# Kernel optimization log

Measured on AMD Instinct MI355X. Metric: run time of the kernel, lower is better.

Reference implementation:

```python
import jax, jax.numpy as jnp
import numpy as np


def setup_inputs() -> dict:
    key = jax.random.key(0)
    ks = jax.random.split(key, 7)
    B, S, D, R = 4, 4096, 1024, 16
    scale = 1.0 / np.sqrt(D)
    return {
        "x": jax.random.normal(ks[0], (B, S, D), dtype=jnp.float32),
        "W_qkv": jax.random.normal(ks[1], (3 * D, D), dtype=jnp.float32) * scale,
        "b_qkv": jax.random.normal(ks[2], (3 * D,), dtype=jnp.float32) * 0.02,
        "W_a_q": jax.random.normal(ks[3], (R, D), dtype=jnp.float32) * scale,
        "W_b_q": jnp.zeros((D, R), dtype=jnp.float32) + jax.random.normal(ks[4], (D, R), dtype=jnp.float32) * 0.02,
        "W_a_v": jax.random.normal(ks[5], (R, D), dtype=jnp.float32) * scale,
        "W_b_v": jax.random.normal(ks[6], (D, R), dtype=jnp.float32) * 0.02,
    }


def reference(x, W_qkv, b_qkv, W_a_q, W_b_q, W_a_v, W_b_v):
    D = W_a_q.shape[1]
    # base qkv projection: [B, S, 3D]
    qkv = jnp.einsum("bsd,ed->bse", x, W_qkv) + b_qkv
    # LoRA branches: x -> [B,S,r] -> [B,S,D]
    q_ba = jnp.einsum("bsr,dr->bsd", jnp.einsum("bsd,rd->bsr", x, W_a_q), W_b_q)
    v_ba = jnp.einsum("bsr,dr->bsd", jnp.einsum("bsd,rd->bsr", x, W_a_v), W_b_v)
    # add into q slice ([:D]) and v slice ([-D:])
    qkv = qkv.at[:, :, :D].add(q_ba)
    qkv = qkv.at[:, :, -D:].add(v_ba)
    return qkv
```

## Files before the change

### kernel.cpp

```cpp
#include <hip/hip_runtime.h>
#include <hip/hip_bf16.h>

typedef __bf16 bf16x4 __attribute__((ext_vector_type(4)));
typedef __bf16 bf16x8 __attribute__((ext_vector_type(8)));
typedef float floatx4 __attribute__((ext_vector_type(4)));

#define GLD16(gp, lp) __builtin_amdgcn_global_load_lds(                      \
    (const __attribute__((address_space(1))) void*)(gp),                     \
    (__attribute__((address_space(3))) void*)(lp), 16, 0, 0)

constexpr int Mdim = 16384;
constexpr int Ndim = 3072;
constexpr int Kdim = 1024;

static __device__ __forceinline__ bf16x8 cvt8(floatx4 lo, floatx4 hi) {
    bf16x8 r;
#pragma unroll
    for (int e = 0; e < 4; ++e) { r[e] = (__bf16)lo[e]; r[e + 4] = (__bf16)hi[e]; }
    return r;
}


__global__ __launch_bounds__(256) void build_weff(
    const float* __restrict__ Wqkv,
    const float* __restrict__ Waq,
    const float* __restrict__ Wbq,
    const float* __restrict__ Wav,
    const float* __restrict__ Wbv,
    __hip_bfloat16* __restrict__ Weff)
{
    const int idx = (blockIdx.x * 256 + threadIdx.x) * 4;
    const int e = idx >> 10;
    const int d = idx & 1023;
    floatx4 v = *(const floatx4*)(Wqkv + idx);
    if (e < 1024) {
#pragma unroll
        for (int r = 0; r < 16; ++r) {
            const float wb = Wbq[e * 16 + r];
            floatx4 wa = *(const floatx4*)(Waq + r * 1024 + d);
#pragma unroll
            for (int q = 0; q < 4; ++q) v[q] += wb * wa[q];
        }
    } else if (e >= 2048) {
        const int e2 = e - 2048;
#pragma unroll
        for (int r = 0; r < 16; ++r) {
            const float wb = Wbv[e2 * 16 + r];
            floatx4 wa = *(const floatx4*)(Wav + r * 1024 + d);
#pragma unroll
            for (int q = 0; q < 4; ++q) v[q] += wb * wa[q];
        }
    }
    bf16x4 o;
#pragma unroll
    for (int q = 0; q < 4; ++q) o[q] = (__bf16)v[q];
    *(bf16x4*)(Weff + idx) = o;
}

__global__ __launch_bounds__(256) void cvt_x(
    const float* __restrict__ x, __hip_bfloat16* __restrict__ xb)
{
    const size_t idx = ((size_t)blockIdx.x * 256 + threadIdx.x) * 8;
    bf16x8 r = cvt8(*(const floatx4*)(x + idx), *(const floatx4*)(x + idx + 4));
    *(bf16x8*)(xb + idx) = r;
}

__global__ __launch_bounds__(512, 2) void gemm_bf16_8ph(
    const __hip_bfloat16* __restrict__ A,
    const __hip_bfloat16* __restrict__ Bw,
    const float* __restrict__ bias,
    float* __restrict__ C)
{
    constexpr int NT = Kdim / 64;
    __shared__ __hip_bfloat16 lds[2][2][256 * 64];

    const int t    = threadIdx.x;
    const int wid  = t >> 6;
    const int lane = t & 63;
    const int wm   = wid >> 2;
    const int wn   = wid & 3;

    constexpr int NWG = (Mdim / 256) * (Ndim / 256);
    const int bid = (blockIdx.x & 7) * (NWG >> 3) + (blockIdx.x >> 3);
    const int bx  = bid % (Ndim / 256);
    const int by  = bid / (Ndim / 256);
    const int m0  = by * 256;
    const int n0  = bx * 256;

    const int srow0 = t >> 3;
    const int scb_s = ((t & 7) * 16) ^ ((srow0 & 7) << 4);

#define STAGE_HALF(G, R0, h, nb_, mat, kt_) do {                               \
    const __hip_bfloat16* _g = (G) + (size_t)((R0) + (h) * 128 + srow0) * Kdim \
                               + (kt_) * 64 + (scb_s >> 1);                    \
    char* _l = (char*)&lds[nb_][mat][0] + (h) * 16384 + t * 16;                \
    GLD16(_g, _l);                                                             \
    GLD16(_g + (size_t)64 * Kdim, _l + 8192);                                  \
} while (0)

    const int fm   = lane & 15;
    const int fk2  = (lane >> 4) * 16;
    const int fxor = (fm & 7) << 4;
    const int cbs0 = fk2 ^ fxor;
    const int cbs1 = (64 + fk2) ^ fxor;

    floatx4 acc[8][4];
#pragma unroll
    for (int i = 0; i < 8; ++i)
#pragma unroll
        for (int j = 0; j < 4; ++j)
            acc[i][j] = (floatx4){0.f, 0.f, 0.f, 0.f};

#define MFMA_QUAD(mq, nq, BQ)                                                  \
    __builtin_amdgcn_s_setprio(1);                                             \
    _Pragma("unroll")                                                          \
    for (int i = 0; i < 4; ++i)                                                \
        _Pragma("unroll")                                                      \
        for (int j = 0; j < 2; ++j) {                                          \
            acc[(mq) * 4 + i][(nq) * 2 + j] =                                  \
                __builtin_amdgcn_mfma_f32_16x16x32_bf16(                       \
                    aq[i][0], BQ[j][0], acc[(mq) * 4 + i][(nq) * 2 + j], 0, 0, 0); \
            acc[(mq) * 4 + i][(nq) * 2 + j] =                                  \
                __builtin_amdgcn_mfma_f32_16x16x32_bf16(                       \
                    aq[i][1], BQ[j][1], acc[(mq) * 4 + i][(nq) * 2 + j], 0, 0, 0); \
        }                                                                      \
    __builtin_amdgcn_s_setprio(0);

    STAGE_HALF(A,  m0, 0, 0, 0, 0);
    STAGE_HALF(A,  m0, 1, 0, 0, 0);
    STAGE_HALF(Bw, n0, 0, 0, 1, 0);
    STAGE_HALF(Bw, n0, 1, 0, 1, 0);

    bf16x8 aq[4][2], bq0[2][2], bq1[2][2];

    for (int kt = 0; kt < NT; ++kt) {
        const int nb = kt & 1;
        const char* Ab = (const char*)&lds[nb][0][0];
        const char* Bb = (const char*)&lds[nb][1][0];

#define LDA8(i, mq, kk) (*(const bf16x8*)(Ab + ((wm * 128 + (mq) * 64 + (i) * 16 + fm) * 128 + cbs##kk)))
#define LDB8(j, nq, kk) (*(const bf16x8*)(Bb + ((wn * 64 + (nq) * 32 + (j) * 16 + fm) * 128 + cbs##kk)))

        if (kt + 1 < NT) {
            STAGE_HALF(A,  m0, 0, nb ^ 1, 0, kt + 1);
            STAGE_HALF(Bw, n0, 0, nb ^ 1, 1, kt + 1);
            asm volatile("s_waitcnt vmcnt(4)" ::: "memory");
        } else {
            asm volatile("s_waitcnt vmcnt(0)" ::: "memory");
        }
        __builtin_amdgcn_s_barrier();
#pragma unroll
        for (int i = 0; i < 4; ++i) { aq[i][0] = LDA8(i, 0, 0); aq[i][1] = LDA8(i, 0, 1); }
#pragma unroll
        for (int j = 0; j < 2; ++j) { bq0[j][0] = LDB8(j, 0, 0); bq0[j][1] = LDB8(j, 0, 1); }
        MFMA_QUAD(0, 0, bq0)
        __builtin_amdgcn_s_barrier();

#pragma unroll
        for (int j = 0; j < 2; ++j) { bq1[j][0] = LDB8(j, 1, 0); bq1[j][1] = LDB8(j, 1, 1); }
        if (kt + 1 < NT) STAGE_HALF(A, m0, 1, nb ^ 1, 0, kt + 1);
        __builtin_amdgcn_s_barrier();
        MFMA_QUAD(0, 1, bq1)
        __builtin_amdgcn_s_barrier();

#pragma unroll
        for (int i = 0; i < 4; ++i) { aq[i][0] = LDA8(i, 1, 0); aq[i][1] = LDA8(i, 1, 1); }
        if (kt + 1 < NT) STAGE_HALF(Bw, n0, 1, nb ^ 1, 1, kt + 1);
        __builtin_amdgcn_s_barrier();
        MFMA_QUAD(1, 0, bq0)
        __builtin_amdgcn_s_barrier();

        MFMA_QUAD(1, 1, bq1)
        __builtin_amdgcn_s_barrier();

#undef LDA8
#undef LDB8
    }

    const int cn = lane & 15;
    const int cm = (lane >> 4) * 4;
    float bv[4];
#pragma unroll
    for (int j = 0; j < 4; ++j)
        bv[j] = bias[n0 + wn * 64 + j * 16 + cn];

#pragma unroll
    for (int mi = 0; mi < 8; ++mi) {
        const int m = m0 + wm * 128 + mi * 16 + cm;
#pragma unroll
        for (int ni = 0; ni < 4; ++ni) {
            const int n = n0 + wn * 64 + ni * 16 + cn;
            const size_t base = (size_t)m * Ndim + n;
#pragma unroll
            for (int r = 0; r < 4; ++r)
                C[base + (size_t)r * Ndim] = acc[mi][ni][r] + bv[ni];
        }
    }
#undef STAGE_HALF
#undef MFMA_QUAD
}


__global__ __launch_bounds__(256, 2) void gemm_bias_f32(
    const float* __restrict__ A, const float* __restrict__ Bw,
    const float* __restrict__ bias, float* __restrict__ C)
{
    constexpr int TK = 32;
    __shared__ __hip_bfloat16 As[128 * TK];
    __shared__ __hip_bfloat16 Bs[128 * TK];

    const int t    = threadIdx.x;
    const int wave = t >> 6;
    const int lane = t & 63;
    const int bx   = blockIdx.x % (Ndim / 128);
    const int by   = blockIdx.x / (Ndim / 128);
    const int m0   = by * 128;
    const int n0   = bx * 128;
    const int wm   = wave >> 1;
    const int wn   = wave & 1;
    const int srow = wave * 16 + (lane >> 2);
    const int scol = (lane & 3) * 8;

    const float* Ag0 = A  + (size_t)(m0 + srow) * Kdim + scol;
    const float* Ag1 = Ag0 + (size_t)64 * Kdim;
    const float* Bg0 = Bw + (size_t)(n0 + srow) * Kdim + scol;
    const float* Bg1 = Bg0 + (size_t)64 * Kdim;

    __hip_bfloat16* Al0 = &As[srow * TK + scol];
    __hip_bfloat16* Al1 = &As[(srow + 64) * TK + scol];
    __hip_bfloat16* Bl0 = &Bs[srow * TK + scol];
    __hip_bfloat16* Bl1 = &Bs[(srow + 64) * TK + scol];

    const int fm = lane & 15;
    const int fk = (lane >> 4) * 8;

    floatx4 acc[4][4];
#pragma unroll
    for (int i = 0; i < 4; ++i)
#pragma unroll
        for (int j = 0; j < 4; ++j)
            acc[i][j] = (floatx4){0.f, 0.f, 0.f, 0.f};

    for (int kt = 0; kt < Kdim; kt += TK) {
        bf16x8 a0 = cvt8(*(const floatx4*)(Ag0 + kt), *(const floatx4*)(Ag0 + kt + 4));
        bf16x8 a1 = cvt8(*(const floatx4*)(Ag1 + kt), *(const floatx4*)(Ag1 + kt + 4));
        bf16x8 b0 = cvt8(*(const floatx4*)(Bg0 + kt), *(const floatx4*)(Bg0 + kt + 4));
        bf16x8 b1 = cvt8(*(const floatx4*)(Bg1 + kt), *(const floatx4*)(Bg1 + kt + 4));
        __syncthreads();
        *(bf16x8*)Al0 = a0;
        *(bf16x8*)Al1 = a1;
        *(bf16x8*)Bl0 = b0;
        *(bf16x8*)Bl1 = b1;
        __syncthreads();

        bf16x8 af[4], bfr[4];
#pragma unroll
        for (int i = 0; i < 4; ++i) {
            af[i]  = *(const bf16x8*)&As[(wm * 64 + i * 16 + fm) * TK + fk];
            bfr[i] = *(const bf16x8*)&Bs[(wn * 64 + i * 16 + fm) * TK + fk];
        }
#pragma unroll
        for (int i = 0; i < 4; ++i)
#pragma unroll
            for (int j = 0; j < 4; ++j)
                acc[i][j] = __builtin_amdgcn_mfma_f32_16x16x32_bf16(af[i], bfr[j], acc[i][j], 0, 0, 0);
    }

    const int cn = lane & 15;
    const int cm = (lane >> 4) * 4;
    float bv[4];
#pragma unroll
    for (int j = 0; j < 4; ++j)
        bv[j] = bias[n0 + wn * 64 + j * 16 + cn];
#pragma unroll
    for (int i = 0; i < 4; ++i) {
        const int m = m0 + wm * 64 + i * 16 + cm;
#pragma unroll
        for (int j = 0; j < 4; ++j) {
            const int n = n0 + wn * 64 + j * 16 + cn;
            const size_t base = (size_t)m * Ndim + n;
#pragma unroll
            for (int r = 0; r < 4; ++r)
                C[base + (size_t)r * Ndim] = acc[i][j][r] + bv[j];
        }
    }
}

__global__ __launch_bounds__(256) void lora_rmw(
    const float* __restrict__ x,
    const float* __restrict__ Waq, const float* __restrict__ Wbq,
    const float* __restrict__ Wav, const float* __restrict__ Wbv,
    float* __restrict__ out)
{
    __shared__ float Pq[64][16];
    __shared__ float Pv[64][16];
    const int t  = threadIdx.x;
    const int m0 = blockIdx.x * 64;
    {
        const int row = t >> 2;
        const int r0  = (t & 3) * 4;
        float accq[4] = {0.f, 0.f, 0.f, 0.f};
        float accv[4] = {0.f, 0.f, 0.f, 0.f};
        const float* xr = x + (size_t)(m0 + row) * Kdim;
        for (int d = 0; d < Kdim; d += 4) {
            floatx4 xv = *(const floatx4*)(xr + d);
#pragma unroll
            for (int rr = 0; rr < 4; ++rr) {
                floatx4 wq = *(const floatx4*)(Waq + (size_t)(r0 + rr) * Kdim + d);
                floatx4 wv = *(const floatx4*)(Wav + (size_t)(r0 + rr) * Kdim + d);
#pragma unroll
                for (int e = 0; e < 4; ++e) {
                    accq[rr] += xv[e] * wq[e];
                    accv[rr] += xv[e] * wv[e];
                }
            }
        }
#pragma unroll
        for (int rr = 0; rr < 4; ++rr) {
            Pq[row][r0 + rr] = accq[rr];
            Pv[row][r0 + rr] = accv[rr];
        }
    }
    __syncthreads();
    const int col  = t * 8;
    const bool isq = col < 1024;
    const int nn0  = isq ? col : col - 1024;
    const int n    = isq ? col : col + 1024;
    const float* Wb = isq ? Wbq : Wbv;
    for (int row = 0; row < 64; ++row) {
        const float* P = isq ? Pq[row] : Pv[row];
        const size_t off = (size_t)(m0 + row) * Ndim + n;
        floatx4 o0 = *(const floatx4*)(out + off);
        floatx4 o1 = *(const floatx4*)(out + off + 4);
#pragma unroll
        for (int i = 0; i < 8; ++i) {
            floatx4 w0 = *(const floatx4*)(Wb + (size_t)(nn0 + i) * 16);
            floatx4 w1 = *(const floatx4*)(Wb + (size_t)(nn0 + i) * 16 + 4);
            floatx4 w2 = *(const floatx4*)(Wb + (size_t)(nn0 + i) * 16 + 8);
            floatx4 w3 = *(const floatx4*)(Wb + (size_t)(nn0 + i) * 16 + 12);
            float s = 0.f;
#pragma unroll
            for (int r = 0; r < 4; ++r)
                s += P[r] * w0[r] + P[r + 4] * w1[r] + P[r + 8] * w2[r] + P[r + 12] * w3[r];
            if (i < 4) o0[i] += s; else o1[i - 4] += s;
        }
        *(floatx4*)(out + off)     = o0;
        *(floatx4*)(out + off + 4) = o1;
    }
}

extern "C" void kernel_launch(void* const* d_in, const int* in_sizes, int n_in,
                              void* d_out, int out_size, void* d_ws, size_t ws_size,
                              hipStream_t stream)
{
    (void)in_sizes; (void)n_in; (void)out_size;
    const float* x    = (const float*)d_in[0];
    const float* Wqkv = (const float*)d_in[1];
    const float* bqkv = (const float*)d_in[2];
    const float* Waq  = (const float*)d_in[3];
    const float* Wbq  = (const float*)d_in[4];
    const float* Wav  = (const float*)d_in[5];
    const float* Wbv  = (const float*)d_in[6];
    float* out = (float*)d_out;

    const size_t WEFF_BYTES = (size_t)Ndim * Kdim * sizeof(__hip_bfloat16);
    const size_t XB_BYTES   = (size_t)Mdim * Kdim * sizeof(__hip_bfloat16);

    if (ws_size >= WEFF_BYTES + XB_BYTES) {
        __hip_bfloat16* Weff = (__hip_bfloat16*)d_ws;
        __hip_bfloat16* xb   = (__hip_bfloat16*)((char*)d_ws + WEFF_BYTES);
        build_weff<<<(Ndim * Kdim / 4) / 256, 256, 0, stream>>>(Wqkv, Waq, Wbq, Wav, Wbv, Weff);
        cvt_x<<<(int)(((size_t)Mdim * Kdim / 8) / 256), 256, 0, stream>>>(x, xb);
        gemm_bf16_8ph<<<(Mdim / 256) * (Ndim / 256), 512, 0, stream>>>(xb, Weff, bqkv, out);
    } else {
        gemm_bias_f32<<<(Mdim / 128) * (Ndim / 128), 256, 0, stream>>>(x, Wqkv, bqkv, out);
        lora_rmw<<<Mdim / 64, 256, 0, stream>>>(x, Waq, Wbq, Wav, Wbv, out);
    }
}
```

Baseline: 366.9 us.

## Restructure GEMM main loop to prefetch B/A halves two stages ahead with fewer barriers

```diff
diff --git a/kernel.cpp b/kernel.cpp
--- a/kernel.cpp
+++ b/kernel.cpp
@@ -65,14 +65,14 @@
     *(bf16x8*)(xb + idx) = r;
 }
 
-__global__ __launch_bounds__(512, 2) void gemm_bf16_8ph(
+__global__ __launch_bounds__(512, 2) void gemm_bf16_v6(
     const __hip_bfloat16* __restrict__ A,
     const __hip_bfloat16* __restrict__ Bw,
     const float* __restrict__ bias,
     float* __restrict__ C)
 {
     constexpr int NT = Kdim / 64;
-    __shared__ __hip_bfloat16 lds[2][2][256 * 64];
+    __shared__ __align__(16) char smem[131072];
 
     const int t    = threadIdx.x;
     const int wid  = t >> 6;
@@ -88,21 +88,23 @@
     const int n0  = bx * 256;
 
     const int srow0 = t >> 3;
-    const int scb_s = ((t & 7) * 16) ^ ((srow0 & 7) << 4);
-
-#define STAGE_HALF(G, R0, h, nb_, mat, kt_) do {                               \
-    const __hip_bfloat16* _g = (G) + (size_t)((R0) + (h) * 128 + srow0) * Kdim \
-                               + (kt_) * 64 + (scb_s >> 1);                    \
-    char* _l = (char*)&lds[nb_][mat][0] + (h) * 16384 + t * 16;                \
-    GLD16(_g, _l);                                                             \
+    const int scb   = ((t & 7) * 16) ^ ((srow0 & 7) << 4);
+    const __hip_bfloat16* Ag = A  + (size_t)(m0 + srow0) * Kdim + (scb >> 1);
+    const __hip_bfloat16* Bg = Bw + (size_t)(n0 + srow0) * Kdim + (scb >> 1);
+
+#define STG(mat, h, kt_, b_) do {                                              \
+    const __hip_bfloat16* _g = ((mat) ? Bg : Ag)                               \
+        + (size_t)((h) * 128) * Kdim + (kt_) * 64;                             \
+    char* _l = smem + (b_) * 65536 + (mat) * 32768 + (h) * 16384 + t * 16;     \
+    GLD16(_g,                     _l);                                         \
     GLD16(_g + (size_t)64 * Kdim, _l + 8192);                                  \
 } while (0)
 
-    const int fm   = lane & 15;
-    const int fk2  = (lane >> 4) * 16;
-    const int fxor = (fm & 7) << 4;
-    const int cbs0 = fk2 ^ fxor;
-    const int cbs1 = (64 + fk2) ^ fxor;
+    const int fm  = lane & 15;
+    const int fk2 = (lane >> 4) * 16;
+    const int fx  = (fm & 7) << 4;
+    const int cb0 = fk2 ^ fx;
+    const int cb1 = (64 + fk2) ^ fx;
 
     floatx4 acc[8][4];
 #pragma unroll
@@ -111,7 +113,7 @@
         for (int j = 0; j < 4; ++j)
             acc[i][j] = (floatx4){0.f, 0.f, 0.f, 0.f};
 
-#define MFMA_QUAD(mq, nq, BQ)                                                  \
+#define MFMA_Q(mq, nq, BQ)                                                     \
     __builtin_amdgcn_s_setprio(1);                                             \
     _Pragma("unroll")                                                          \
     for (int i = 0; i < 4; ++i)                                                \
@@ -119,62 +121,69 @@
         for (int j = 0; j < 2; ++j) {                                          \
             acc[(mq) * 4 + i][(nq) * 2 + j] =                                  \
                 __builtin_amdgcn_mfma_f32_16x16x32_bf16(                       \
-                    aq[i][0], BQ[j][0], acc[(mq) * 4 + i][(nq) * 2 + j], 0, 0, 0); \
+                    aq[i][0], BQ[j][0], acc[(mq) * 4 + i][(nq) * 2 + j], 0,0,0);\
             acc[(mq) * 4 + i][(nq) * 2 + j] =                                  \
                 __builtin_amdgcn_mfma_f32_16x16x32_bf16(                       \
-                    aq[i][1], BQ[j][1], acc[(mq) * 4 + i][(nq) * 2 + j], 0, 0, 0); \
+                    aq[i][1], BQ[j][1], acc[(mq) * 4 + i][(nq) * 2 + j], 0,0,0);\
         }                                                                      \
     __builtin_amdgcn_s_setprio(0);
 
-    STAGE_HALF(A,  m0, 0, 0, 0, 0);
-    STAGE_HALF(A,  m0, 1, 0, 0, 0);
-    STAGE_HALF(Bw, n0, 0, 0, 1, 0);
-    STAGE_HALF(Bw, n0, 1, 0, 1, 0);
+    STG(0, 0, 0, 0); STG(0, 1, 0, 0); STG(1, 0, 0, 0); STG(1, 1, 0, 0);
+    STG(1, 0, 1, 1); STG(0, 0, 1, 1);
 
     bf16x8 aq[4][2], bq0[2][2], bq1[2][2];
 
     for (int kt = 0; kt < NT; ++kt) {
-        const int nb = kt & 1;
-        const char* Ab = (const char*)&lds[nb][0][0];
-        const char* Bb = (const char*)&lds[nb][1][0];
-
-#define LDA8(i, mq, kk) (*(const bf16x8*)(Ab + ((wm * 128 + (mq) * 64 + (i) * 16 + fm) * 128 + cbs##kk)))
-#define LDB8(j, nq, kk) (*(const bf16x8*)(Bb + ((wn * 64 + (nq) * 32 + (j) * 16 + fm) * 128 + cbs##kk)))
+        const int b = kt & 1;
+        const char* Ab = smem + b * 65536;
+        const char* Bb = Ab + 32768;
 
         if (kt + 1 < NT) {
-            STAGE_HALF(A,  m0, 0, nb ^ 1, 0, kt + 1);
-            STAGE_HALF(Bw, n0, 0, nb ^ 1, 1, kt + 1);
-            asm volatile("s_waitcnt vmcnt(4)" ::: "memory");
+            STG(0, 1, kt + 1, b ^ 1);
+            asm volatile("s_waitcnt vmcnt(6)" ::: "memory");
         } else {
             asm volatile("s_waitcnt vmcnt(0)" ::: "memory");
         }
         __builtin_amdgcn_s_barrier();
-#pragma unroll
-        for (int i = 0; i < 4; ++i) { aq[i][0] = LDA8(i, 0, 0); aq[i][1] = LDA8(i, 0, 1); }
-#pragma unroll
-        for (int j = 0; j < 2; ++j) { bq0[j][0] = LDB8(j, 0, 0); bq0[j][1] = LDB8(j, 0, 1); }
-        MFMA_QUAD(0, 0, bq0)
+        __builtin_amdgcn_sched_barrier(0x8);
+#pragma unroll
+        for (int i = 0; i < 4; ++i) {
+            const char* ar = Ab + (wm * 128 + i * 16 + fm) * 128;
+            aq[i][0] = *(const bf16x8*)(ar + cb0);
+            aq[i][1] = *(const bf16x8*)(ar + cb1);
+        }
+#pragma unroll
+        for (int j = 0; j < 2; ++j) {
+            const char* br = Bb + (wn * 64 + j * 16 + fm) * 128;
+            bq0[j][0] = *(const bf16x8*)(br + cb0);
+            bq0[j][1] = *(const bf16x8*)(br + cb1);
+        }
+        MFMA_Q(0, 0, bq0)
+
+#pragma unroll
+        for (int j = 0; j < 2; ++j) {
+            const char* br = Bb + (wn * 64 + 32 + j * 16 + fm) * 128;
+            bq1[j][0] = *(const bf16x8*)(br + cb0);
+            bq1[j][1] = *(const bf16x8*)(br + cb1);
+        }
+        if (kt + 1 < NT) STG(1, 1, kt + 1, b ^ 1);
+        MFMA_Q(0, 1, bq1)
         __builtin_amdgcn_s_barrier();
-
-#pragma unroll
-        for (int j = 0; j < 2; ++j) { bq1[j][0] = LDB8(j, 1, 0); bq1[j][1] = LDB8(j, 1, 1); }
-        if (kt + 1 < NT) STAGE_HALF(A, m0, 1, nb ^ 1, 0, kt + 1);
+        __builtin_amdgcn_sched_barrier(0x108);
+
+#pragma unroll
+        for (int i = 0; i < 4; ++i) {
+            const char* ar = Ab + (wm * 128 + 64 + i * 16 + fm) * 128;
+            aq[i][0] = *(const bf16x8*)(ar + cb0);
+            aq[i][1] = *(const bf16x8*)(ar + cb1);
+        }
+        if (kt + 2 < NT) STG(1, 0, kt + 2, b);
+        MFMA_Q(1, 0, bq0)
         __builtin_amdgcn_s_barrier();
-        MFMA_QUAD(0, 1, bq1)
-        __builtin_amdgcn_s_barrier();
-
-#pragma unroll
-        for (int i = 0; i < 4; ++i) { aq[i][0] = LDA8(i, 1, 0); aq[i][1] = LDA8(i, 1, 1); }
-        if (kt + 1 < NT) STAGE_HALF(Bw, n0, 1, nb ^ 1, 1, kt + 1);
-        __builtin_amdgcn_s_barrier();
-        MFMA_QUAD(1, 0, bq0)
-        __builtin_amdgcn_s_barrier();
-
-        MFMA_QUAD(1, 1, bq1)
-        __builtin_amdgcn_s_barrier();
-
-#undef LDA8
-#undef LDB8
+        __builtin_amdgcn_sched_barrier(0x108);
+
+        if (kt + 2 < NT) STG(0, 0, kt + 2, b);
+        MFMA_Q(1, 1, bq1)
     }
 
     const int cn = lane & 15;
@@ -196,8 +205,8 @@
                 C[base + (size_t)r * Ndim] = acc[mi][ni][r] + bv[ni];
         }
     }
-#undef STAGE_HALF
-#undef MFMA_QUAD
+#undef STG
+#undef MFMA_Q
 }
 
 
@@ -371,7 +380,7 @@
         __hip_bfloat16* xb   = (__hip_bfloat16*)((char*)d_ws + WEFF_BYTES);
         build_weff<<<(Ndim * Kdim / 4) / 256, 256, 0, stream>>>(Wqkv, Waq, Wbq, Wav, Wbv, Weff);
         cvt_x<<<(int)(((size_t)Mdim * Kdim / 8) / 256), 256, 0, stream>>>(x, xb);
-        gemm_bf16_8ph<<<(Mdim / 256) * (Ndim / 256), 512, 0, stream>>>(xb, Weff, bqkv, out);
+        gemm_bf16_v6<<<(Mdim / 256) * (Ndim / 256), 512, 0, stream>>>(xb, Weff, bqkv, out);
     } else {
         gemm_bias_f32<<<(Mdim / 128) * (Ndim / 128), 256, 0, stream>>>(x, Wqkv, bqkv, out);
         lora_rmw<<<Mdim / 64, 256, 0, stream>>>(x, Waq, Wbq, Wav, Wbv, out);
```

Measured after the change: 360.3 us. No clear change (-1.8%).
